# Optimization experiments

Hardware: AMD Instinct MI355X
Metric: run time of the kernel (lower is better)

Reference implementation:

```python
import jax, jax.numpy as jnp
import numpy as np

B, T, C = 8, 2048, 1024      # batch, timesteps, input_dim
G, E = 2, 320                # groups_dim, entries_dim
EMB = 512                    # emb_dim
D = EMB // G                 # true_emb_dim per group


def setup_inputs() -> dict:
    key = jax.random.key(0)
    k1, k2, k3 = jax.random.split(key, 3)
    X = jax.random.normal(k1, (B, T, C), dtype=jnp.float32)
    # nn.Linear(input_dim, G*E): weight (out,in) ~ N(0,1), bias zeros
    W = jax.random.normal(k2, (G * E, C), dtype=jnp.float32)
    b = jnp.zeros((G * E,), dtype=jnp.float32)
    # codebook Parameter(1, G*E, D) ~ U[0,1); stored squeezed as (G*E, D)
    codebook = jax.random.uniform(k3, (G * E, D), dtype=jnp.float32)
    return {"X": X, "W": W, "b": b, "codebook": codebook}


def reference(X, W, b, codebook):
    # Eval-mode forward of VectorQuantization (time_first=True).
    nB, nT, _ = X.shape
    logits = jnp.einsum("btc,kc->btk", X, W) + b           # (B, T, G*E)
    # Faithful to source: view (B,T,G*E) as (B*G, T*E) and argmax over last dim
    flat = logits.reshape(nB * G, nT * E)                   # (B*G, T*E)
    k = jnp.argmax(flat, axis=-1)                           # (B*G,)
    hard = jax.nn.one_hot(k, nT * E, dtype=logits.dtype)    # (B*G, T*E)
    q = hard.reshape(nB * nT, G, E)                         # (B*T, G, E)
    # (one-hot * codebook).sum over entries == per-group gather
    cb = codebook.reshape(G, E, D)                          # (G, E, D)
    out = jnp.einsum("nge,ged->ngd", q, cb)                 # (B*T, G, D)
    return out.reshape(nB, nT, G * D)                       # (B, T, emb_dim)
```

## Files before the change

kernel.cpp:

```cpp
#include <hip/hip_runtime.h>
#include <stdint.h>

#define CC    1024
#define EE    320
#define KN    640
#define DD    256
#define MTOT  16384
#define WK2   2048

typedef __attribute__((ext_vector_type(8))) short short8;
typedef __attribute__((ext_vector_type(4))) float f32x4;

__device__ __forceinline__ unsigned int f32_orderable(float x) {
    unsigned int b = __float_as_uint(x);
    return (b & 0x80000000u) ? ~b : (b | 0x80000000u);
}

__device__ __forceinline__ unsigned short bf16_rne(float x) {
    unsigned int u = __float_as_uint(x);
    return (unsigned short)((u + 0x7FFFu + ((u >> 16) & 1u)) >> 16);
}

__device__ __forceinline__ void cvt_hilo8(float4 a, float4 b, short8& hi, short8& lo) {
    float x[8] = {a.x, a.y, a.z, a.w, b.x, b.y, b.z, b.w};
#pragma unroll
    for (int j = 0; j < 8; j++) {
        unsigned int u  = __float_as_uint(x[j]);
        unsigned int v  = u + 0x8000u;
        float hif       = __uint_as_float(v & 0xFFFF0000u);
        float lof       = x[j] - hif;
        unsigned int lu = __float_as_uint(lof) + 0x8000u;
        hi[j] = (short)(v >> 16);
        lo[j] = (short)(lu >> 16);
    }
}

__device__ __forceinline__ void gload_lds16(const void* g, void* l) {
    __builtin_amdgcn_global_load_lds(
        (const __attribute__((address_space(1))) unsigned int*)g,
        (__attribute__((address_space(3))) unsigned int*)l,
        16, 0, 0);
}

__global__ void init_slots_kernel(unsigned long long* __restrict__ slots) {
    if (threadIdx.x < 16) slots[threadIdx.x] = 0ull;
}

__global__ __launch_bounds__(256)
void convert_kernel(const float* __restrict__ X, const float* __restrict__ W,
                    unsigned short* __restrict__ A2F, unsigned short* __restrict__ B2,
                    unsigned long long* __restrict__ slots) {
    const int bid = blockIdx.x;
    if (bid < 8192) {
        int gtid = bid * 256 + threadIdx.x;
        int lane = gtid & 63;
        int kc   = (gtid >> 6) & 31;
        int mb   = gtid >> 11;
        int row  = mb * 16 + (lane & 15);
        int col  = kc * 32 + ((lane >> 4) << 3);
        const float* p = X + (size_t)row * CC + col;
        float4 v0 = *(const float4*)p;
        float4 v1 = *(const float4*)(p + 4);
        short8 hi, lo;
        cvt_hilo8(v0, v1, hi, lo);
        size_t base = ((size_t)(mb * 32 + kc) * 2) * 512 + lane * 8;
        *(short8*)(A2F + base)       = hi;
        *(short8*)(A2F + base + 512) = lo;
    } else {
        if (bid == 8192 && threadIdx.x < 16) slots[threadIdx.x] = 0ull;
        int i4 = (bid - 8192) * 256 + threadIdx.x;
        int m = i4 >> 8;
        int k = (i4 & 255) * 4;
        float4 v = ((const float4*)W)[i4];
        ushort4 hi, lo;
        hi.x = bf16_rne(v.x); lo.x = bf16_rne(v.x - __uint_as_float((unsigned)hi.x << 16));
        hi.y = bf16_rne(v.y); lo.y = bf16_rne(v.y - __uint_as_float((unsigned)hi.y << 16));
        hi.z = bf16_rne(v.z); lo.z = bf16_rne(v.z - __uint_as_float((unsigned)hi.z << 16));
        hi.w = bf16_rne(v.w); lo.w = bf16_rne(v.w - __uint_as_float((unsigned)hi.w << 16));
        *(ushort4*)(B2 + (size_t)m * WK2 + k)        = hi;
        *(ushort4*)(B2 + (size_t)m * WK2 + 1024 + k) = lo;
    }
}

__global__ __launch_bounds__(256, 3)
void gemm_argmax_mfma(const unsigned short* __restrict__ A2F,
                      const unsigned short* __restrict__ B2,
                      const float* __restrict__ bias,
                      unsigned long long* __restrict__ slots) {
    __shared__ unsigned short Bs[2][2][128 * 32];
    __shared__ unsigned long long red[4];

    const int tid  = threadIdx.x;
    const int lane = tid & 63;
    const int wave = tid >> 6;

    const int l   = blockIdx.x;
    const int xcd = l & 7;
    const int w   = l >> 3;
    const int mt  = xcd * 16 + w / 5;
    const int nt  = w % 5;
    const int m0 = mt * 128;
    const int n0 = nt * 128;

    const int wm = (wave >> 1) * 64;
    const int wn = (wave & 1) * 64;
    const int fr = lane & 15;
    const int q  = lane >> 4;

    const unsigned short* Ap[4];
#pragma unroll
    for (int t = 0; t < 4; t++)
        Ap[t] = A2F + ((size_t)(((m0 + wm) >> 4) + t) * 32) * 1024 + lane * 8;

    int soff[2];
#pragma unroll
    for (int c = 0; c < 2; c++) {
        int rt   = wave * 32 + c * 16 + (lane >> 2);
        int slot = ((lane & 3) - (rt >> 1)) & 3;
        soff[c]  = (n0 + rt) * WK2 + slot * 8;
    }
    const int ldsb0 = (wave * 32) * 64;
    const int ldsb1 = (wave * 32 + 16) * 64;
    const int fbase = (wn + fr) * 32 + ((q + (fr >> 1)) & 3) * 8;

    f32x4 acc[4][4] = {};

#pragma unroll
    for (int c = 0; c < 2; c++) {
        const unsigned short* sp = B2 + soff[c];
        int lb = c ? ldsb1 : ldsb0;
        gload_lds16(sp,        (char*)Bs[0][0] + lb);
        gload_lds16(sp + 1024, (char*)Bs[0][1] + lb);
    }

    for (int it = 0; it < 32; it++) {
        const int buf = it & 1;
        __syncthreads();

        short8 ah[4], al[4];
#pragma unroll
        for (int t = 0; t < 4; t++) {
            ah[t] = *(const short8*)(Ap[t]);
            al[t] = *(const short8*)(Ap[t] + 512);
            Ap[t] += 1024;
        }
        if (it < 31) {
            const int k1 = (it + 1) * 32;
#pragma unroll
            for (int c = 0; c < 2; c++) {
                const unsigned short* sp = B2 + soff[c] + k1;
                int lb = c ? ldsb1 : ldsb0;
                gload_lds16(sp,        (char*)Bs[buf ^ 1][0] + lb);
                gload_lds16(sp + 1024, (char*)Bs[buf ^ 1][1] + lb);
            }
        }
        short8 bh[4], bl[4];
#pragma unroll
        for (int t = 0; t < 4; t++) {
            bh[t] = *(const short8*)&Bs[buf][0][fbase + t * 512];
            bl[t] = *(const short8*)&Bs[buf][1][fbase + t * 512];
        }
#pragma unroll
        for (int ti = 0; ti < 4; ti++)
#pragma unroll
            for (int tj = 0; tj < 4; tj++)
                acc[ti][tj] = __builtin_amdgcn_mfma_f32_16x16x32_bf16(ah[ti], bh[tj], acc[ti][tj], 0, 0, 0);
#pragma unroll
        for (int ti = 0; ti < 4; ti++)
#pragma unroll
            for (int tj = 0; tj < 4; tj++)
                acc[ti][tj] = __builtin_amdgcn_mfma_f32_16x16x32_bf16(al[ti], bh[tj], acc[ti][tj], 0, 0, 0);
#pragma unroll
        for (int ti = 0; ti < 4; ti++)
#pragma unroll
            for (int tj = 0; tj < 4; tj++)
                acc[ti][tj] = __builtin_amdgcn_mfma_f32_16x16x32_bf16(ah[ti], bl[tj], acc[ti][tj], 0, 0, 0);
    }

    float bias4[4];
#pragma unroll
    for (int tj = 0; tj < 4; tj++) bias4[tj] = bias[n0 + wn + tj * 16 + (lane & 15)];

    unsigned long long best = 0ull;
#pragma unroll
    for (int ti = 0; ti < 4; ti++) {
#pragma unroll
        for (int r = 0; r < 4; r++) {
            int m  = m0 + wm + ti * 16 + (lane >> 4) * 4 + r;
            int tl = m & 1023;
#pragma unroll
            for (int tj = 0; tj < 4; tj++) {
                int n = n0 + wn + tj * 16 + (lane & 15);
                float v = acc[ti][tj][r] + bias4[tj];
                unsigned int c = (unsigned int)(tl * KN + n);
                unsigned long long p =
                    ((unsigned long long)f32_orderable(v) << 32) |
                    (unsigned long long)(~c);
                if (p > best) best = p;
            }
        }
    }
#pragma unroll
    for (int off = 32; off > 0; off >>= 1) {
        unsigned long long o = __shfl_down(best, off, 64);
        if (o > best) best = o;
    }
    if (lane == 0) red[wave] = best;
    __syncthreads();
    if (tid == 0) {
        unsigned long long b = red[0];
        for (int wv = 1; wv < 4; wv++) if (red[wv] > b) b = red[wv];
        atomicMax(slots + (m0 >> 10), b);
    }
}

__global__ __launch_bounds__(256)
void zs_kernel(const unsigned long long* __restrict__ slots,
               const float* __restrict__ codebook,
               float4* __restrict__ out4) {
    int i4 = blockIdx.x * 256 + threadIdx.x;
    int n  = i4 >> 7;
    int c4 = i4 & 127;
    int b  = n >> 11;
    int h  = (n >> 10) & 1;
    unsigned long long p = slots[b * 2 + h];
    unsigned int c = ~(unsigned int)(p & 0xFFFFFFFFull);
    int tl = (int)(c / KN);
    int kg = (int)(c % KN);
    int nstar = b * 2048 + h * 1024 + tl;
    int g = kg / EE;
    float4 v = make_float4(0.f, 0.f, 0.f, 0.f);
    if (n == nstar && (c4 >> 6) == g)
        v = ((const float4*)codebook)[kg * 64 + (c4 & 63)];
    out4[i4] = v;
}

#define BM 128
#define BN 64
#define BK 32
#define LDA (BM + 4)
#define LDB (BN + 4)

__global__ __launch_bounds__(128)
void gemm_argmax_f32(const float* __restrict__ X, const float* __restrict__ W,
                     const float* __restrict__ bias,
                     unsigned long long* __restrict__ slots) {
    __shared__ float As[BK][LDA];
    __shared__ float Bs[BK][LDB];
    const int tid = threadIdx.x;
    const int m0 = blockIdx.y * BM;
    const int n0 = blockIdx.x * BN;
    const int tx = tid & 7, ty = tid >> 3;
    float acc[8][8];
#pragma unroll
    for (int i = 0; i < 8; i++)
#pragma unroll
        for (int j = 0; j < 8; j++) acc[i][j] = 0.0f;
    const int lm = tid >> 3, lk = (tid & 7) * 4;
    const float* Xb = X + (size_t)m0 * CC;
    const float* Wb = W + (size_t)n0 * CC;
    for (int k0 = 0; k0 < CC; k0 += BK) {
#pragma unroll
        for (int r = 0; r < 8; r++) {
            int m = r * 16 + lm;
            float4 v = *(const float4*)(Xb + (size_t)m * CC + k0 + lk);
            As[lk + 0][m] = v.x; As[lk + 1][m] = v.y; As[lk + 2][m] = v.z; As[lk + 3][m] = v.w;
        }
#pragma unroll
        for (int r = 0; r < 4; r++) {
            int m = r * 16 + lm;
            float4 v = *(const float4*)(Wb + (size_t)m * CC + k0 + lk);
            Bs[lk + 0][m] = v.x; Bs[lk + 1][m] = v.y; Bs[lk + 2][m] = v.z; Bs[lk + 3][m] = v.w;
        }
        __syncthreads();
#pragma unroll
        for (int kk = 0; kk < BK; kk++) {
            float4 a0 = *(const float4*)&As[kk][ty * 8];
            float4 a1 = *(const float4*)&As[kk][ty * 8 + 4];
            float4 b0 = *(const float4*)&Bs[kk][tx * 8];
            float4 b1 = *(const float4*)&Bs[kk][tx * 8 + 4];
            float a[8] = {a0.x, a0.y, a0.z, a0.w, a1.x, a1.y, a1.z, a1.w};
            float b[8] = {b0.x, b0.y, b0.z, b0.w, b1.x, b1.y, b1.z, b1.w};
#pragma unroll
            for (int i = 0; i < 8; i++)
#pragma unroll
                for (int j = 0; j < 8; j++) acc[i][j] = fmaf(a[i], b[j], acc[i][j]);
        }
        __syncthreads();
    }
    unsigned long long best = 0ull;
#pragma unroll
    for (int i = 0; i < 8; i++) {
        int mg = m0 + ty * 8 + i;
        int tl = mg & 1023;
#pragma unroll
        for (int j = 0; j < 8; j++) {
            int kg = n0 + tx * 8 + j;
            float v = acc[i][j] + bias[kg];
            unsigned int c = (unsigned int)(tl * KN + kg);
            unsigned long long p = ((unsigned long long)f32_orderable(v) << 32) |
                                   (unsigned long long)(~c);
            if (p > best) best = p;
        }
    }
#pragma unroll
    for (int off = 32; off > 0; off >>= 1) {
        unsigned long long o = __shfl_down(best, off, 64);
        if (o > best) best = o;
    }
    __shared__ unsigned long long red2[2];
    if ((tid & 63) == 0) red2[tid >> 6] = best;
    __syncthreads();
    if (tid == 0) {
        unsigned long long b0 = red2[0], b1 = red2[1];
        atomicMax(slots + (m0 >> 10), b0 > b1 ? b0 : b1);
    }
}

extern "C" void kernel_launch(void* const* d_in, const int* in_sizes, int n_in,
                              void* d_out, int out_size, void* d_ws, size_t ws_size,
                              hipStream_t stream) {
    const float* X        = (const float*)d_in[0];
    const float* W        = (const float*)d_in[1];
    const float* bias     = (const float*)d_in[2];
    const float* codebook = (const float*)d_in[3];
    float* out = (float*)d_out;

    unsigned long long* slots = (unsigned long long*)d_ws;
    const size_t A_off   = 256;
    const size_t A_bytes = (size_t)MTOT * CC * 2 * 2;
    const size_t B_off   = A_off + A_bytes;
    const size_t B_bytes = (size_t)KN * WK2 * 2;
    const size_t need = B_off + B_bytes;

    if (ws_size >= need) {
        unsigned short* A2F = (unsigned short*)((char*)d_ws + A_off);
        unsigned short* B2  = (unsigned short*)((char*)d_ws + B_off);
        hipLaunchKernelGGL(convert_kernel, dim3(8192 + 640), dim3(256), 0, stream,
                           X, W, A2F, B2, slots);
        hipLaunchKernelGGL(gemm_argmax_mfma, dim3(640), dim3(256), 0, stream,
                           A2F, B2, bias, slots);
    } else {
        hipLaunchKernelGGL(init_slots_kernel, dim3(1), dim3(64), 0, stream, slots);
        hipLaunchKernelGGL(gemm_argmax_f32, dim3(KN / BN, MTOT / BM), dim3(128), 0, stream,
                           X, W, bias, slots);
    }

    int n4 = out_size / 4;
    hipLaunchKernelGGL(zs_kernel, dim3(n4 / 256), dim3(256), 0, stream,
                       slots, codebook, (float4*)out);
}
```

Baseline: 186.5 us.

## Fuse output zeroing and codebook scatter into GEMM-argmax kernel with last-block finish

The separate zero-and-scatter kernel is folded into the MFMA GEMM kernel. Each block writes its share of the zeroed output with nontemporal stores before the main loop. The last block to arrive, detected by an atomic counter, reads the 16 argmax slots and copies the chosen codebook rows into the output. The A-fragment loads are also software-pipelined into register double buffers, so the next K-step's global loads are issued before the current step's MFMAs. This removes one kernel launch and overlaps the output writes with GEMM work, at the cost of more registers, a threadfence and a serialized tail in one block.

```diff
diff --git a/kernel.cpp b/kernel.cpp
--- a/kernel.cpp
+++ b/kernel.cpp
@@ -7,6 +7,8 @@
 #define DD    256
 #define MTOT  16384
 #define WK2   2048
+#define NBLK  640
+#define OUT4  2097152
 
 typedef __attribute__((ext_vector_type(8))) short short8;
 typedef __attribute__((ext_vector_type(4))) float f32x4;
@@ -43,7 +45,7 @@
 }
 
 __global__ void init_slots_kernel(unsigned long long* __restrict__ slots) {
-    if (threadIdx.x < 16) slots[threadIdx.x] = 0ull;
+    if (threadIdx.x < 17) slots[threadIdx.x] = 0ull;
 }
 
 __global__ __launch_bounds__(256)
@@ -67,7 +69,7 @@
         *(short8*)(A2F + base)       = hi;
         *(short8*)(A2F + base + 512) = lo;
     } else {
-        if (bid == 8192 && threadIdx.x < 16) slots[threadIdx.x] = 0ull;
+        if (bid == 8192 && threadIdx.x < 17) slots[threadIdx.x] = 0ull;
         int i4 = (bid - 8192) * 256 + threadIdx.x;
         int m = i4 >> 8;
         int k = (i4 & 255) * 4;
@@ -86,9 +88,14 @@
 void gemm_argmax_mfma(const unsigned short* __restrict__ A2F,
                       const unsigned short* __restrict__ B2,
                       const float* __restrict__ bias,
-                      unsigned long long* __restrict__ slots) {
+                      const float* __restrict__ codebook,
+                      float* __restrict__ out,
+                      unsigned long long* __restrict__ slots,
+                      unsigned int* __restrict__ counter) {
     __shared__ unsigned short Bs[2][2][128 * 32];
     __shared__ unsigned long long red[4];
+    __shared__ unsigned int done_s;
+    __shared__ unsigned long long s16[16];
 
     const int tid  = threadIdx.x;
     const int lane = tid & 63;
@@ -124,6 +131,7 @@
     const int fbase = (wn + fr) * 32 + ((q + (fr >> 1)) & 3) * 8;
 
     f32x4 acc[4][4] = {};
+    short8 a0h[4], a0l[4], a1h[4], a1l[4];
 
 #pragma unroll
     for (int c = 0; c < 2; c++) {
@@ -132,50 +140,73 @@
         gload_lds16(sp,        (char*)Bs[0][0] + lb);
         gload_lds16(sp + 1024, (char*)Bs[0][1] + lb);
     }
-
-    for (int it = 0; it < 32; it++) {
-        const int buf = it & 1;
-        __syncthreads();
-
-        short8 ah[4], al[4];
-#pragma unroll
-        for (int t = 0; t < 4; t++) {
-            ah[t] = *(const short8*)(Ap[t]);
-            al[t] = *(const short8*)(Ap[t] + 512);
-            Ap[t] += 1024;
-        }
-        if (it < 31) {
-            const int k1 = (it + 1) * 32;
-#pragma unroll
-            for (int c = 0; c < 2; c++) {
-                const unsigned short* sp = B2 + soff[c] + k1;
-                int lb = c ? ldsb1 : ldsb0;
-                gload_lds16(sp,        (char*)Bs[buf ^ 1][0] + lb);
-                gload_lds16(sp + 1024, (char*)Bs[buf ^ 1][1] + lb);
-            }
-        }
-        short8 bh[4], bl[4];
-#pragma unroll
-        for (int t = 0; t < 4; t++) {
-            bh[t] = *(const short8*)&Bs[buf][0][fbase + t * 512];
-            bl[t] = *(const short8*)&Bs[buf][1][fbase + t * 512];
-        }
-#pragma unroll
-        for (int ti = 0; ti < 4; ti++)
-#pragma unroll
-            for (int tj = 0; tj < 4; tj++)
-                acc[ti][tj] = __builtin_amdgcn_mfma_f32_16x16x32_bf16(ah[ti], bh[tj], acc[ti][tj], 0, 0, 0);
-#pragma unroll
-        for (int ti = 0; ti < 4; ti++)
-#pragma unroll
-            for (int tj = 0; tj < 4; tj++)
-                acc[ti][tj] = __builtin_amdgcn_mfma_f32_16x16x32_bf16(al[ti], bh[tj], acc[ti][tj], 0, 0, 0);
-#pragma unroll
-        for (int ti = 0; ti < 4; ti++)
-#pragma unroll
-            for (int tj = 0; tj < 4; tj++)
-                acc[ti][tj] = __builtin_amdgcn_mfma_f32_16x16x32_bf16(ah[ti], bl[tj], acc[ti][tj], 0, 0, 0);
-    }
+#pragma unroll
+    for (int t = 0; t < 4; t++) {
+        a0h[t] = *(const short8*)(Ap[t]);
+        a0l[t] = *(const short8*)(Ap[t] + 512);
+        Ap[t] += 1024;
+    }
+
+    {
+        f32x4 z = {0.f, 0.f, 0.f, 0.f};
+        int idx = l * 256 + tid;
+#pragma unroll
+        for (int r = 0; r < 13; r++) {
+            if (idx < OUT4) __builtin_nontemporal_store(z, (f32x4*)out + idx);
+            idx += NBLK * 256;
+        }
+    }
+
+#define STEP(BUF, CURH, CURL, NXTH, NXTL, IT)                                    \
+    {                                                                            \
+        __syncthreads();                                                         \
+        if ((IT) < 31) {                                                         \
+            const int k1 = ((IT) + 1) * 32;                                      \
+            _Pragma("unroll")                                                    \
+            for (int c = 0; c < 2; c++) {                                        \
+                const unsigned short* sp = B2 + soff[c] + k1;                    \
+                int lb = c ? ldsb1 : ldsb0;                                      \
+                gload_lds16(sp,        (char*)Bs[(BUF) ^ 1][0] + lb);            \
+                gload_lds16(sp + 1024, (char*)Bs[(BUF) ^ 1][1] + lb);            \
+            }                                                                    \
+            _Pragma("unroll")                                                    \
+            for (int t = 0; t < 4; t++) {                                        \
+                NXTH[t] = *(const short8*)(Ap[t]);                               \
+                NXTL[t] = *(const short8*)(Ap[t] + 512);                         \
+                Ap[t] += 1024;                                                   \
+            }                                                                    \
+        }                                                                        \
+        short8 bh[4], bl[4];                                                     \
+        _Pragma("unroll")                                                        \
+        for (int t = 0; t < 4; t++) {                                            \
+            bh[t] = *(const short8*)&Bs[BUF][0][fbase + t * 512];                \
+            bl[t] = *(const short8*)&Bs[BUF][1][fbase + t * 512];                \
+        }                                                                        \
+        _Pragma("unroll")                                                        \
+        for (int ti = 0; ti < 4; ti++)                                           \
+            _Pragma("unroll")                                                    \
+            for (int tj = 0; tj < 4; tj++)                                       \
+                acc[ti][tj] = __builtin_amdgcn_mfma_f32_16x16x32_bf16(           \
+                    CURH[ti], bh[tj], acc[ti][tj], 0, 0, 0);                     \
+        _Pragma("unroll")                                                        \
+        for (int ti = 0; ti < 4; ti++)                                           \
+            _Pragma("unroll")                                                    \
+            for (int tj = 0; tj < 4; tj++)                                       \
+                acc[ti][tj] = __builtin_amdgcn_mfma_f32_16x16x32_bf16(           \
+                    CURL[ti], bh[tj], acc[ti][tj], 0, 0, 0);                     \
+        _Pragma("unroll")                                                        \
+        for (int ti = 0; ti < 4; ti++)                                           \
+            _Pragma("unroll")                                                    \
+            for (int tj = 0; tj < 4; tj++)                                       \
+                acc[ti][tj] = __builtin_amdgcn_mfma_f32_16x16x32_bf16(           \
+                    CURH[ti], bl[tj], acc[ti][tj], 0, 0, 0);                     \
+    }
+
+    for (int it2 = 0; it2 < 16; it2++) {
+        STEP(0, a0h, a0l, a1h, a1l, it2 * 2)
+        STEP(1, a1h, a1l, a0h, a0l, it2 * 2 + 1)
+    }
+#undef STEP
 
     float bias4[4];
 #pragma unroll
@@ -211,6 +242,27 @@
         unsigned long long b = red[0];
         for (int wv = 1; wv < 4; wv++) if (red[wv] > b) b = red[wv];
         atomicMax(slots + (m0 >> 10), b);
+        __threadfence();
+        done_s = atomicAdd(counter, 1u);
+    }
+    __syncthreads();
+
+    if (done_s == NBLK - 1) {
+        if (tid < 16) s16[tid] = atomicAdd(slots + tid, 0ull);
+        __syncthreads();
+        int rr  = tid >> 4;
+        int seg = tid & 15;
+        unsigned long long p = s16[rr];
+        unsigned int c = ~(unsigned int)(p & 0xFFFFFFFFull);
+        int tl = (int)(c / KN);
+        int kg = (int)(c % KN);
+        int b  = rr >> 1, h = rr & 1;
+        int nstar = b * 2048 + h * 1024 + tl;
+        int g = kg / EE;
+        const float4* src = (const float4*)(codebook + (size_t)kg * DD) + seg * 4;
+        float4* dst = (float4*)(out + (size_t)nstar * 512 + (size_t)g * DD) + seg * 4;
+#pragma unroll
+        for (int j = 0; j < 4; j++) dst[j] = src[j];
     }
 }
 
@@ -246,7 +298,7 @@
                      const float* __restrict__ bias,
                      unsigned long long* __restrict__ slots) {
     __shared__ float As[BK][LDA];
-    __shared__ float Bs[BK][LDB];
+    __shared__ float Bsm[BK][LDB];
     const int tid = threadIdx.x;
     const int m0 = blockIdx.y * BM;
     const int n0 = blockIdx.x * BN;
@@ -270,15 +322,15 @@
         for (int r = 0; r < 4; r++) {
             int m = r * 16 + lm;
             float4 v = *(const float4*)(Wb + (size_t)m * CC + k0 + lk);
-            Bs[lk + 0][m] = v.x; Bs[lk + 1][m] = v.y; Bs[lk + 2][m] = v.z; Bs[lk + 3][m] = v.w;
+            Bsm[lk + 0][m] = v.x; Bsm[lk + 1][m] = v.y; Bsm[lk + 2][m] = v.z; Bsm[lk + 3][m] = v.w;
         }
         __syncthreads();
 #pragma unroll
         for (int kk = 0; kk < BK; kk++) {
             float4 a0 = *(const float4*)&As[kk][ty * 8];
             float4 a1 = *(const float4*)&As[kk][ty * 8 + 4];
-            float4 b0 = *(const float4*)&Bs[kk][tx * 8];
-            float4 b1 = *(const float4*)&Bs[kk][tx * 8 + 4];
+            float4 b0 = *(const float4*)&Bsm[kk][tx * 8];
+            float4 b1 = *(const float4*)&Bsm[kk][tx * 8 + 4];
             float a[8] = {a0.x, a0.y, a0.z, a0.w, a1.x, a1.y, a1.z, a1.w};
             float b[8] = {b0.x, b0.y, b0.z, b0.w, b1.x, b1.y, b1.z, b1.w};
 #pragma unroll
@@ -327,6 +379,7 @@
     float* out = (float*)d_out;
 
     unsigned long long* slots = (unsigned long long*)d_ws;
+    unsigned int* counter = (unsigned int*)(slots + 16);
     const size_t A_off   = 256;
     const size_t A_bytes = (size_t)MTOT * CC * 2 * 2;
     const size_t B_off   = A_off + A_bytes;
@@ -338,15 +391,13 @@
         unsigned short* B2  = (unsigned short*)((char*)d_ws + B_off);
         hipLaunchKernelGGL(convert_kernel, dim3(8192 + 640), dim3(256), 0, stream,
                            X, W, A2F, B2, slots);
-        hipLaunchKernelGGL(gemm_argmax_mfma, dim3(640), dim3(256), 0, stream,
-                           A2F, B2, bias, slots);
+        hipLaunchKernelGGL(gemm_argmax_mfma, dim3(NBLK), dim3(256), 0, stream,
+                           A2F, B2, bias, codebook, out, slots, counter);
     } else {
         hipLaunchKernelGGL(init_slots_kernel, dim3(1), dim3(64), 0, stream, slots);
         hipLaunchKernelGGL(gemm_argmax_f32, dim3(KN / BN, MTOT / BM), dim3(128), 0, stream,
                            X, W, bias, slots);
-    }
-
-    int n4 = out_size / 4;
-    hipLaunchKernelGGL(zs_kernel, dim3(n4 / 256), dim3(256), 0, stream,
-                       slots, codebook, (float4*)out);
-}
+        hipLaunchKernelGGL(zs_kernel, dim3(OUT4 / 256), dim3(256), 0, stream,
+                           slots, codebook, (float4*)out);
+    }
+}
```

New measurement: 190.9 us. +2.4%, slower.
